# Optimization experiments

Measured on AMD Instinct MI355X. Metric: run time of the kernel, lower is better.

The kernel has to match this reference:

```python
import jax, jax.numpy as jnp
import numpy as np

N = 50000    # nodes
E = 800000   # edges (avg degree 16)
H = 4        # attention heads
IN = 128     # input feature size
HID = 128    # hidden size per head
OUT = 64     # output size per head
GAT_SLOPE = 0.2   # DGL GATConv internal LeakyReLU slope
ACT_SLOPE = 0.01  # nn.LeakyReLU default slope


def _lrelu(x, s):
    return jnp.where(x >= 0, x, s * x)


def _gat_conv(x, src, dst, W, attn_l, attn_r, bias, heads, out_dim):
    """DGL GATConv (feat_drop disabled for deterministic reference).
    x: [N, F_in] -> out: [N, heads, out_dim]"""
    z = (x @ W).reshape(N, heads, out_dim)                 # [N,H,D]
    el = jnp.sum(z * attn_l, axis=-1)                      # [N,H]
    er = jnp.sum(z * attn_r, axis=-1)                      # [N,H]
    e = _lrelu(el[src] + er[dst], GAT_SLOPE)               # [E,H]
    # edge softmax over incoming edges of each dst node (numerically stable)
    emax = jax.ops.segment_max(e, dst, num_segments=N)     # [N,H]
    ex = jnp.exp(e - emax[dst])                            # [E,H]
    esum = jax.ops.segment_sum(ex, dst, num_segments=N)    # [N,H]
    alpha = ex / esum[dst]                                 # [E,H]
    msg = alpha[:, :, None] * z[src]                       # [E,H,D]
    out = jax.ops.segment_sum(msg, dst, num_segments=N)    # [N,H,D]
    return out + bias.reshape(1, heads, out_dim)


def setup_inputs() -> dict:
    key = jax.random.key(0)
    ks = jax.random.split(key, 20)
    def nrm(k, shape, scale=0.05):
        return jax.random.normal(k, shape, dtype=jnp.float32) * scale
    return {
        "n_feat": jax.random.normal(ks[0], (N, IN), dtype=jnp.float32),
        "src": jax.random.randint(ks[1], (E,), 0, N),
        "dst": jax.random.randint(ks[2], (E,), 0, N),
        # input GATConv: IN -> HID x H
        "g0_W": nrm(ks[3], (IN, H * HID)),
        "g0_al": nrm(ks[4], (H, HID)),
        "g0_ar": nrm(ks[5], (H, HID)),
        "g0_b": jnp.zeros((H * HID,), jnp.float32),
        "d0_W": nrm(ks[6], (HID, H * HID)),
        "d0_b": jnp.zeros((HID,), jnp.float32),
        # middle GATConv: HID -> HID x H
        "g1_W": nrm(ks[7], (HID, H * HID)),
        "g1_al": nrm(ks[8], (H, HID)),
        "g1_ar": nrm(ks[9], (H, HID)),
        "g1_b": jnp.zeros((H * HID,), jnp.float32),
        "d1_W": nrm(ks[10], (HID, H * HID)),
        "d1_b": jnp.zeros((HID,), jnp.float32),
        # output GATConv: HID -> OUT x H
        "g2_W": nrm(ks[11], (HID, H * OUT)),
        "g2_al": nrm(ks[12], (H, OUT)),
        "g2_ar": nrm(ks[13], (H, OUT)),
        "g2_b": jnp.zeros((H * OUT,), jnp.float32),
    }


def reference(n_feat, src, dst,
              g0_W, g0_al, g0_ar, g0_b, d0_W, d0_b,
              g1_W, g1_al, g1_ar, g1_b, d1_W, d1_b,
              g2_W, g2_al, g2_ar, g2_b):
    # input GAT + dense
    h = _gat_conv(n_feat, src, dst, g0_W, g0_al, g0_ar, g0_b, H, HID)  # [N,H,HID]
    h = _lrelu(h, ACT_SLOPE).reshape(N, H * HID)
    h = _lrelu(h @ d0_W.T + d0_b, ACT_SLOPE)                            # [N,HID]
    # middle GAT + dense
    h = _gat_conv(h, src, dst, g1_W, g1_al, g1_ar, g1_b, H, HID)
    h = _lrelu(h, ACT_SLOPE).reshape(N, H * HID)
    h = _lrelu(h @ d1_W.T + d1_b, ACT_SLOPE)                            # [N,HID]
    # output GAT, mean over heads
    h = _gat_conv(h, src, dst, g2_W, g2_al, g2_ar, g2_b, H, OUT)        # [N,H,OUT]
    h = _lrelu(h, ACT_SLOPE)
    h = jnp.mean(h, axis=-2)                                            # [N,OUT]
    h = _lrelu(h, ACT_SLOPE)
    return h
```

## Files before the change

### kernel.cpp

```cpp
#include <hip/hip_runtime.h>

#define NN 50000
#define EE 800000
#define HH 4

typedef __attribute__((ext_vector_type(8))) short short8v;
typedef __attribute__((ext_vector_type(4))) float f32x4;
typedef __attribute__((ext_vector_type(8))) unsigned short ushort8v;
typedef __attribute__((ext_vector_type(4))) unsigned short ushort4v;

__device__ __forceinline__ float b2f(unsigned short u) {
    return __uint_as_float(((unsigned int)u) << 16);
}
__device__ __forceinline__ unsigned short f2b(float f) {
    unsigned int x = __float_as_uint(f);
    x += 0x7fffu + ((x >> 16) & 1u);
    return (unsigned short)(x >> 16);
}

template<int WR, bool ACT, int WEL>
__global__ __launch_bounds__(256) void mgemm_k(
    const unsigned short* __restrict__ A, const unsigned short* __restrict__ Bt,
    const float* __restrict__ bias, unsigned short* __restrict__ C,
    const float* __restrict__ al, const float* __restrict__ ar,
    float* __restrict__ el, float* __restrict__ er,
    int M, int N, int K, float slope)
{
    constexpr int BM = 64 * WR;
    __shared__ unsigned short As[BM * 72];
    __shared__ unsigned short Bs[128 * 72];
    const int t   = threadIdx.x;
    const int m0  = blockIdx.y * BM;
    const int n0  = blockIdx.x * 128;
    const int w   = t >> 6;
    const int l   = t & 63;
    const int lr  = l & 15;
    const int lk8 = (l >> 4) * 8;
    const int wbase = w * 16 * WR;

    f32x4 acc[WR][8];
    #pragma unroll
    for (int rr = 0; rr < WR; ++rr)
        #pragma unroll
        for (int i = 0; i < 8; ++i) acc[rr][i] = (f32x4)0.f;

    for (int k0 = 0; k0 < K; k0 += 64) {
        #pragma unroll
        for (int cc = 0; cc < 2 * WR; ++cc) {
            int c = t + cc * 256;
            int row = c >> 3, seg = (c & 7) * 8;
            int gm = m0 + row;
            short8v v = (short8v)0;
            if (gm < M)
                v = *reinterpret_cast<const short8v*>(&A[(size_t)gm * K + k0 + seg]);
            *reinterpret_cast<short8v*>(&As[row * 72 + seg]) = v;
        }
        #pragma unroll
        for (int cc = 0; cc < 4; ++cc) {
            int c = t + cc * 256;
            int row = c >> 3, seg = (c & 7) * 8;
            short8v v = *reinterpret_cast<const short8v*>(
                &Bt[(size_t)(n0 + row) * K + k0 + seg]);
            *reinterpret_cast<short8v*>(&Bs[row * 72 + seg]) = v;
        }
        __syncthreads();
        #pragma unroll
        for (int kk = 0; kk < 64; kk += 32) {
            short8v a[WR];
            #pragma unroll
            for (int rr = 0; rr < WR; ++rr)
                a[rr] = *reinterpret_cast<const short8v*>(
                    &As[(wbase + rr * 16 + lr) * 72 + kk + lk8]);
            #pragma unroll
            for (int nb = 0; nb < 8; ++nb) {
                short8v b = *reinterpret_cast<const short8v*>(
                    &Bs[(nb * 16 + lr) * 72 + kk + lk8]);
                #pragma unroll
                for (int rr = 0; rr < WR; ++rr)
                    acc[rr][nb] = __builtin_amdgcn_mfma_f32_16x16x32_bf16(
                        a[rr], b, acc[rr][nb], 0, 0, 0);
            }
        }
        __syncthreads();
    }

    if (WEL > 0) {
        const int nbh = (WEL == 1) ? 8 : 4;
        const int Dd  = (WEL == 1) ? 128 : 64;
        #pragma unroll
        for (int hh = 0; hh < WEL; ++hh) {
            int head = (WEL == 1) ? blockIdx.x : blockIdx.x * 2 + hh;
            #pragma unroll
            for (int rr = 0; rr < WR; ++rr) {
                float pl[4] = {}, pr[4] = {};
                #pragma unroll
                for (int nb = 0; nb < nbh; ++nb) {
                    float alv = al[head * Dd + nb * 16 + lr];
                    float arv = ar[head * Dd + nb * 16 + lr];
                    #pragma unroll
                    for (int r = 0; r < 4; ++r) {
                        float z = acc[rr][hh * nbh + nb][r];
                        pl[r] = fmaf(z, alv, pl[r]);
                        pr[r] = fmaf(z, arv, pr[r]);
                    }
                }
                #pragma unroll
                for (int r = 0; r < 4; ++r) {
                    #pragma unroll
                    for (int o = 1; o < 16; o <<= 1) {
                        pl[r] += __shfl_xor(pl[r], o);
                        pr[r] += __shfl_xor(pr[r], o);
                    }
                }
                if (lr == 0) {
                    #pragma unroll
                    for (int r = 0; r < 4; ++r) {
                        int gm = m0 + wbase + rr * 16 + (l >> 4) * 4 + r;
                        if (gm < M) {
                            el[gm * HH + head] = pl[r];
                            er[gm * HH + head] = pr[r];
                        }
                    }
                }
            }
        }
    }

    #pragma unroll
    for (int rr = 0; rr < WR; ++rr) {
        #pragma unroll
        for (int nb = 0; nb < 8; ++nb) {
            #pragma unroll
            for (int r = 0; r < 4; ++r) {
                int gm = m0 + wbase + rr * 16 + (l >> 4) * 4 + r;
                int gn = n0 + nb * 16 + lr;
                if (gm < M) {
                    float v = acc[rr][nb][r];
                    if (ACT) { v += bias[gn]; v = v >= 0.f ? v : slope * v; }
                    C[(size_t)gm * N + gn] = f2b(v);
                }
            }
        }
    }
}

__global__ void tr_k(const float* __restrict__ W, unsigned short* __restrict__ Wt,
                     int K, int N)
{
    int idx = blockIdx.x * blockDim.x + threadIdx.x;
    if (idx >= K * N) return;
    int n = idx / K, k = idx - n * K;
    Wt[idx] = f2b(W[(size_t)k * N + n]);
}

__global__ void cast_k(const float* __restrict__ x, unsigned short* __restrict__ y,
                       int n4)
{
    int i = blockIdx.x * blockDim.x + threadIdx.x;
    if (i >= n4) return;
    float4 v = reinterpret_cast<const float4*>(x)[i];
    ushort4v u;
    u[0] = f2b(v.x); u[1] = f2b(v.y); u[2] = f2b(v.z); u[3] = f2b(v.w);
    reinterpret_cast<ushort4v*>(y)[i] = u;
}

__global__ void hist_k(const int* __restrict__ dst, int* __restrict__ cnt)
{
    int i = blockIdx.x * blockDim.x + threadIdx.x;
    if (i < EE) atomicAdd(&cnt[dst[i]], 1);
}

#define SCAN_B 196
__global__ __launch_bounds__(256) void scan1_k(const int* __restrict__ cnt,
                                               int* __restrict__ offs,
                                               int* __restrict__ bsum)
{
    __shared__ int sh[256];
    int b = blockIdx.x, t = threadIdx.x, i = b * 256 + t;
    int v = (i < NN) ? cnt[i] : 0;
    sh[t] = v;
    __syncthreads();
    #pragma unroll
    for (int o = 1; o < 256; o <<= 1) {
        int add = (t >= o) ? sh[t - o] : 0;
        __syncthreads();
        sh[t] += add;
        __syncthreads();
    }
    if (i < NN) offs[i] = sh[t] - v;
    if (t == 255) bsum[b] = sh[t];
}

__global__ __launch_bounds__(256) void scan2_k(int* __restrict__ bsum)
{
    __shared__ int sh[256];
    int t = threadIdx.x;
    int v = (t < SCAN_B) ? bsum[t] : 0;
    sh[t] = v;
    __syncthreads();
    #pragma unroll
    for (int o = 1; o < 256; o <<= 1) {
        int add = (t >= o) ? sh[t - o] : 0;
        __syncthreads();
        sh[t] += add;
        __syncthreads();
    }
    if (t < SCAN_B) bsum[t] = sh[t] - v;
}

__global__ __launch_bounds__(256) void scan3_k(int* __restrict__ offs,
                                               const int* __restrict__ bsum)
{
    int b = blockIdx.x, t = threadIdx.x, i = b * 256 + t;
    if (i < NN) offs[i] += bsum[b];
    if (i == NN - 1) offs[NN] = EE;
}

__global__ void scatter_k(const int* __restrict__ src, const int* __restrict__ dst,
                          const int* __restrict__ offs, int* __restrict__ cursor,
                          int* __restrict__ srcs_sorted)
{
    int i = blockIdx.x * blockDim.x + threadIdx.x;
    if (i >= EE) return;
    int d = dst[i];
    int p = offs[d] + atomicAdd(&cursor[d], 1);
    srcs_sorted[p] = src[i];
}

template<int D, bool MEAN>
__global__ __launch_bounds__(256) void agg2_k(
    const unsigned short* __restrict__ zb, const float* __restrict__ el,
    const float* __restrict__ er, const int* __restrict__ offs,
    const int* __restrict__ srcs, const float* __restrict__ bias,
    unsigned short* __restrict__ outb, float* __restrict__ outf)
{
    constexpr int HD  = HH * D;
    constexpr int EPL = HD / 64;
    typedef __attribute__((ext_vector_type(EPL))) unsigned short uvec;
    int n = blockIdx.x * 4 + (threadIdx.x >> 6);
    if (n >= NN) return;
    int lane = threadIdx.x & 63;
    int h = lane >> 4;
    int beg = offs[n];
    int cnt_e = offs[n + 1] - beg;
    float erh = er[n * HH + h];

    float acc[EPL] = {};
    float wsum = 0.f;

    if (cnt_e > 0) {
        auto LD = [&](int idx, uvec& v, float& elv) {
            int e = idx < cnt_e ? idx : cnt_e - 1;
            int s = srcs[beg + e];
            elv = el[s * HH + h];
            v = *reinterpret_cast<const uvec*>(&zb[(size_t)s * HD + lane * EPL]);
        };
        auto PROC = [&](const uvec& v, float elv) {
            float x = elv + erh;
            x = x >= 0.f ? x : 0.2f * x;
            float ex = __expf(x);
            wsum += ex;
            #pragma unroll
            for (int j = 0; j < EPL; ++j)
                acc[j] = fmaf(ex, b2f(v[j]), acc[j]);
        };
        uvec v0, v1, v2, v3;
        float e0, e1, e2, e3;
        LD(0, v0, e0); LD(1, v1, e1); LD(2, v2, e2); LD(3, v3, e3);
        for (int c0 = 0; c0 < cnt_e; c0 += 4) {
            PROC(v0, e0); LD(c0 + 4, v0, e0);
            if (c0 + 1 < cnt_e) { PROC(v1, e1); } LD(c0 + 5, v1, e1);
            if (c0 + 2 < cnt_e) { PROC(v2, e2); } LD(c0 + 6, v2, e2);
            if (c0 + 3 < cnt_e) { PROC(v3, e3); } LD(c0 + 7, v3, e3);
        }
    }
    float inv = wsum > 0.f ? 1.f / wsum : 0.f;

    float vv[EPL];
    #pragma unroll
    for (int j = 0; j < EPL; ++j) {
        float v = acc[j] * inv + bias[h * D + (lane & 15) * EPL + j];
        vv[j] = v >= 0.f ? v : 0.01f * v;
    }

    if (!MEAN) {
        uvec u;
        #pragma unroll
        for (int j = 0; j < EPL; ++j) u[j] = f2b(vv[j]);
        *reinterpret_cast<uvec*>(&outb[(size_t)n * HD + lane * EPL]) = u;
    } else {
        #pragma unroll
        for (int j = 0; j < EPL; ++j) {
            float s = vv[j];
            s += __shfl_xor(s, 16);
            s += __shfl_xor(s, 32);
            s *= 0.25f;
            vv[j] = s >= 0.f ? s : 0.01f * s;
        }
        if (lane < 16) {
            float* op = outf + (size_t)n * D + lane * EPL;
            #pragma unroll
            for (int j = 0; j < EPL; j += 4)
                *reinterpret_cast<float4*>(op + j) =
                    make_float4(vv[j], vv[j + 1], vv[j + 2], vv[j + 3]);
        }
    }
}

extern "C" void kernel_launch(void* const* d_in, const int* in_sizes, int n_in,
                              void* d_out, int out_size, void* d_ws, size_t ws_size,
                              hipStream_t stream)
{
    const float* n_feat = (const float*)d_in[0];
    const int*   src    = (const int*)d_in[1];
    const int*   dst    = (const int*)d_in[2];
    const float* g0_W  = (const float*)d_in[3];
    const float* g0_al = (const float*)d_in[4];
    const float* g0_ar = (const float*)d_in[5];
    const float* g0_b  = (const float*)d_in[6];
    const float* d0_W  = (const float*)d_in[7];
    const float* d0_b  = (const float*)d_in[8];
    const float* g1_W  = (const float*)d_in[9];
    const float* g1_al = (const float*)d_in[10];
    const float* g1_ar = (const float*)d_in[11];
    const float* g1_b  = (const float*)d_in[12];
    const float* d1_W  = (const float*)d_in[13];
    const float* d1_b  = (const float*)d_in[14];
    const float* g2_W  = (const float*)d_in[15];
    const float* g2_al = (const float*)d_in[16];
    const float* g2_ar = (const float*)d_in[17];
    const float* g2_b  = (const float*)d_in[18];

    char* ws = (char*)d_ws;
    size_t off = 0;
    auto alloc = [&](size_t bytes) {
        void* p = ws + off;
        off += (bytes + 255) & ~(size_t)255;
        return p;
    };
    unsigned short* zB   = (unsigned short*)alloc((size_t)NN * 512 * 2);
    unsigned short* hB   = (unsigned short*)alloc((size_t)NN * 512 * 2);
    unsigned short* hC   = (unsigned short*)alloc((size_t)NN * 128 * 2);
    unsigned short* xF   = (unsigned short*)alloc((size_t)NN * 128 * 2);
    unsigned short* g0t  = (unsigned short*)alloc(512 * 128 * 2);
    unsigned short* g1t  = (unsigned short*)alloc(512 * 128 * 2);
    unsigned short* g2t  = (unsigned short*)alloc(256 * 128 * 2);
    unsigned short* d0t  = (unsigned short*)alloc(128 * 512 * 2);
    unsigned short* d1t  = (unsigned short*)alloc(128 * 512 * 2);
    float*          el   = (float*)alloc((size_t)NN * HH * 4);
    float*          er   = (float*)alloc((size_t)NN * HH * 4);
    int*            cnt  = (int*)alloc((size_t)NN * 4);
    int*            curs = (int*)alloc((size_t)NN * 4);
    int*            offs = (int*)alloc((size_t)(NN + 1) * 4);
    int*            srcs = (int*)alloc((size_t)EE * 4);
    int*            bsum = (int*)alloc(256 * 4);

    hipMemsetAsync(cnt, 0, (size_t)NN * 4, stream);
    hipMemsetAsync(curs, 0, (size_t)NN * 4, stream);
    hist_k<<<(EE + 255) / 256, 256, 0, stream>>>(dst, cnt);
    scan1_k<<<SCAN_B, 256, 0, stream>>>(cnt, offs, bsum);
    scan2_k<<<1, 256, 0, stream>>>(bsum);
    scan3_k<<<SCAN_B, 256, 0, stream>>>(offs, bsum);
    scatter_k<<<(EE + 255) / 256, 256, 0, stream>>>(src, dst, offs, curs, srcs);

    cast_k<<<(NN * 128 / 4 + 255) / 256, 256, 0, stream>>>(n_feat, xF, NN * 128 / 4);
    cast_k<<<(128 * 512 / 4 + 255) / 256, 256, 0, stream>>>(d0_W, d0t, 128 * 512 / 4);
    cast_k<<<(128 * 512 / 4 + 255) / 256, 256, 0, stream>>>(d1_W, d1t, 128 * 512 / 4);
    tr_k<<<(128 * 512 + 255) / 256, 256, 0, stream>>>(g0_W, g0t, 128, 512);
    tr_k<<<(128 * 512 + 255) / 256, 256, 0, stream>>>(g1_W, g1t, 128, 512);
    tr_k<<<(128 * 256 + 255) / 256, 256, 0, stream>>>(g2_W, g2t, 128, 256);

    const int MT   = (NN + 63) / 64;
    const int MT2  = (NN + 127) / 128;
    const int NODB = (NN + 3) / 4;

    mgemm_k<2, false, 1><<<dim3(4, MT2), 256, 0, stream>>>(
        xF, g0t, nullptr, zB, g0_al, g0_ar, el, er, NN, 512, 128, 0.f);
    agg2_k<128, false><<<NODB, 256, 0, stream>>>(zB, el, er, offs, srcs, g0_b,
                                                 hB, nullptr);
    mgemm_k<1, true, 0><<<dim3(1, MT), 256, 0, stream>>>(
        hB, d0t, d0_b, hC, nullptr, nullptr, nullptr, nullptr, NN, 128, 512, 0.01f);

    mgemm_k<2, false, 1><<<dim3(4, MT2), 256, 0, stream>>>(
        hC, g1t, nullptr, zB, g1_al, g1_ar, el, er, NN, 512, 128, 0.f);
    agg2_k<128, false><<<NODB, 256, 0, stream>>>(zB, el, er, offs, srcs, g1_b,
                                                 hB, nullptr);
    mgemm_k<1, true, 0><<<dim3(1, MT), 256, 0, stream>>>(
        hB, d1t, d1_b, hC, nullptr, nullptr, nullptr, nullptr, NN, 128, 512, 0.01f);

    mgemm_k<2, false, 2><<<dim3(2, MT2), 256, 0, stream>>>(
        hC, g2t, nullptr, zB, g2_al, g2_ar, el, er, NN, 256, 128, 0.f);
    agg2_k<64, true><<<NODB, 256, 0, stream>>>(zB, el, er, offs, srcs, g2_b,
                                               nullptr, (float*)d_out);
}
```

Measured before the change: 570.7 us.

## Register-prefetch GEMM tiles, fuse prep kernels, use larger M tile for dense GEMMs

The GEMM kernel now loads the next K-slice of A and B into registers while the current slice is being consumed from shared memory, so global-load latency overlaps with MFMA work. The six separate cast/transpose launches are merged into one prep kernel that branches on a flat index, cutting launch overhead. The two dense (K=512) GEMMs switch from WR=1 to WR=2, using 128-row tiles and fewer blocks. The prefetch adds register pressure, which may lower occupancy, and the larger tiles halve the block count for the dense GEMMs.

```diff
diff --git a/kernel.cpp b/kernel.cpp
--- a/kernel.cpp
+++ b/kernel.cpp
@@ -6,7 +6,6 @@
 
 typedef __attribute__((ext_vector_type(8))) short short8v;
 typedef __attribute__((ext_vector_type(4))) float f32x4;
-typedef __attribute__((ext_vector_type(8))) unsigned short ushort8v;
 typedef __attribute__((ext_vector_type(4))) unsigned short ushort4v;
 
 __device__ __forceinline__ float b2f(unsigned short u) {
@@ -27,6 +26,7 @@
     int M, int N, int K, float slope)
 {
     constexpr int BM = 64 * WR;
+    constexpr int NA = 2 * WR;
     __shared__ unsigned short As[BM * 72];
     __shared__ unsigned short Bs[128 * 72];
     const int t   = threadIdx.x;
@@ -44,26 +44,41 @@
         #pragma unroll
         for (int i = 0; i < 8; ++i) acc[rr][i] = (f32x4)0.f;
 
-    for (int k0 = 0; k0 < K; k0 += 64) {
-        #pragma unroll
-        for (int cc = 0; cc < 2 * WR; ++cc) {
+    short8v ra[NA], rb[4];
+    auto LOAD = [&](int k0) {
+        #pragma unroll
+        for (int cc = 0; cc < NA; ++cc) {
             int c = t + cc * 256;
             int row = c >> 3, seg = (c & 7) * 8;
             int gm = m0 + row;
-            short8v v = (short8v)0;
+            ra[cc] = (short8v)0;
             if (gm < M)
-                v = *reinterpret_cast<const short8v*>(&A[(size_t)gm * K + k0 + seg]);
-            *reinterpret_cast<short8v*>(&As[row * 72 + seg]) = v;
+                ra[cc] = *reinterpret_cast<const short8v*>(
+                    &A[(size_t)gm * K + k0 + seg]);
         }
         #pragma unroll
         for (int cc = 0; cc < 4; ++cc) {
             int c = t + cc * 256;
             int row = c >> 3, seg = (c & 7) * 8;
-            short8v v = *reinterpret_cast<const short8v*>(
+            rb[cc] = *reinterpret_cast<const short8v*>(
                 &Bt[(size_t)(n0 + row) * K + k0 + seg]);
-            *reinterpret_cast<short8v*>(&Bs[row * 72 + seg]) = v;
-        }
-        __syncthreads();
+        }
+    };
+
+    LOAD(0);
+    for (int k0 = 0; k0 < K; k0 += 64) {
+        #pragma unroll
+        for (int cc = 0; cc < NA; ++cc) {
+            int c = t + cc * 256;
+            *reinterpret_cast<short8v*>(&As[(c >> 3) * 72 + (c & 7) * 8]) = ra[cc];
+        }
+        #pragma unroll
+        for (int cc = 0; cc < 4; ++cc) {
+            int c = t + cc * 256;
+            *reinterpret_cast<short8v*>(&Bs[(c >> 3) * 72 + (c & 7) * 8]) = rb[cc];
+        }
+        __syncthreads();
+        if (k0 + 64 < K) LOAD(k0 + 64);
         #pragma unroll
         for (int kk = 0; kk < 64; kk += 32) {
             short8v a[WR];
@@ -144,24 +159,35 @@
     }
 }
 
-__global__ void tr_k(const float* __restrict__ W, unsigned short* __restrict__ Wt,
-                     int K, int N)
-{
-    int idx = blockIdx.x * blockDim.x + threadIdx.x;
-    if (idx >= K * N) return;
-    int n = idx / K, k = idx - n * K;
-    Wt[idx] = f2b(W[(size_t)k * N + n]);
-}
-
-__global__ void cast_k(const float* __restrict__ x, unsigned short* __restrict__ y,
-                       int n4)
+#define PREP_T 1796608
+__global__ __launch_bounds__(256) void prep_k(
+    const float* __restrict__ n_feat, const float* __restrict__ d0_W,
+    const float* __restrict__ d1_W, const float* __restrict__ g0_W,
+    const float* __restrict__ g1_W, const float* __restrict__ g2_W,
+    unsigned short* __restrict__ xF, unsigned short* __restrict__ d0t,
+    unsigned short* __restrict__ d1t, unsigned short* __restrict__ g0t,
+    unsigned short* __restrict__ g1t, unsigned short* __restrict__ g2t)
 {
     int i = blockIdx.x * blockDim.x + threadIdx.x;
-    if (i >= n4) return;
-    float4 v = reinterpret_cast<const float4*>(x)[i];
-    ushort4v u;
-    u[0] = f2b(v.x); u[1] = f2b(v.y); u[2] = f2b(v.z); u[3] = f2b(v.w);
-    reinterpret_cast<ushort4v*>(y)[i] = u;
+    if (i >= PREP_T) return;
+    if (i < 1632768) {
+        const float* src; unsigned short* dstp; int j;
+        if (i < 1600000)      { src = n_feat; dstp = xF;  j = i; }
+        else if (i < 1616384) { src = d0_W;   dstp = d0t; j = i - 1600000; }
+        else                  { src = d1_W;   dstp = d1t; j = i - 1616384; }
+        float4 v = reinterpret_cast<const float4*>(src)[j];
+        ushort4v u;
+        u[0] = f2b(v.x); u[1] = f2b(v.y); u[2] = f2b(v.z); u[3] = f2b(v.w);
+        reinterpret_cast<ushort4v*>(dstp)[j] = u;
+    } else {
+        const float* W; unsigned short* Wt; int j, K = 128;
+        if (i < 1698304)      { W = g0_W; Wt = g0t; j = i - 1632768; }
+        else if (i < 1763840) { W = g1_W; Wt = g1t; j = i - 1698304; }
+        else                  { W = g2_W; Wt = g2t; j = i - 1763840; }
+        int N = (i < 1763840) ? 512 : 256;
+        int n = j / K, k = j - n * K;
+        Wt[j] = f2b(W[(size_t)k * N + n]);
+    }
 }
 
 __global__ void hist_k(const int* __restrict__ dst, int* __restrict__ cnt)
@@ -362,15 +388,9 @@
     scan2_k<<<1, 256, 0, stream>>>(bsum);
     scan3_k<<<SCAN_B, 256, 0, stream>>>(offs, bsum);
     scatter_k<<<(EE + 255) / 256, 256, 0, stream>>>(src, dst, offs, curs, srcs);
-
-    cast_k<<<(NN * 128 / 4 + 255) / 256, 256, 0, stream>>>(n_feat, xF, NN * 128 / 4);
-    cast_k<<<(128 * 512 / 4 + 255) / 256, 256, 0, stream>>>(d0_W, d0t, 128 * 512 / 4);
-    cast_k<<<(128 * 512 / 4 + 255) / 256, 256, 0, stream>>>(d1_W, d1t, 128 * 512 / 4);
-    tr_k<<<(128 * 512 + 255) / 256, 256, 0, stream>>>(g0_W, g0t, 128, 512);
-    tr_k<<<(128 * 512 + 255) / 256, 256, 0, stream>>>(g1_W, g1t, 128, 512);
-    tr_k<<<(128 * 256 + 255) / 256, 256, 0, stream>>>(g2_W, g2t, 128, 256);
-
-    const int MT   = (NN + 63) / 64;
+    prep_k<<<(PREP_T + 255) / 256, 256, 0, stream>>>(
+        n_feat, d0_W, d1_W, g0_W, g1_W, g2_W, xF, d0t, d1t, g0t, g1t, g2t);
+
     const int MT2  = (NN + 127) / 128;
     const int NODB = (NN + 3) / 4;
 
@@ -378,14 +398,14 @@
         xF, g0t, nullptr, zB, g0_al, g0_ar, el, er, NN, 512, 128, 0.f);
     agg2_k<128, false><<<NODB, 256, 0, stream>>>(zB, el, er, offs, srcs, g0_b,
                                                  hB, nullptr);
-    mgemm_k<1, true, 0><<<dim3(1, MT), 256, 0, stream>>>(
+    mgemm_k<2, true, 0><<<dim3(1, MT2), 256, 0, stream>>>(
         hB, d0t, d0_b, hC, nullptr, nullptr, nullptr, nullptr, NN, 128, 512, 0.01f);
 
     mgemm_k<2, false, 1><<<dim3(4, MT2), 256, 0, stream>>>(
         hC, g1t, nullptr, zB, g1_al, g1_ar, el, er, NN, 512, 128, 0.f);
     agg2_k<128, false><<<NODB, 256, 0, stream>>>(zB, el, er, offs, srcs, g1_b,
                                                  hB, nullptr);
-    mgemm_k<1, true, 0><<<dim3(1, MT), 256, 0, stream>>>(
+    mgemm_k<2, true, 0><<<dim3(1, MT2), 256, 0, stream>>>(
         hB, d1t, d1_b, hC, nullptr, nullptr, nullptr, nullptr, NN, 128, 512, 0.01f);
 
     mgemm_k<2, false, 2><<<dim3(2, MT2), 256, 0, stream>>>(
```

New measurement: 546.5 us. 1.04x faster.
